# Kernel tuning notes

Measured on AMD Instinct MI355X. Metric: run time of the kernel, lower is better.

Reference implementation:

```python
import jax, jax.numpy as jnp
import numpy as np

W_PRIMAL, W_DUAL, W_STAT, W_COMP = 0.1, 0.1, 0.6, 0.2

B_ = 64
M_PER = 2048
N_PER = 2048
E = 8388608
SUM_M = B_ * M_PER
SUM_N = B_ * N_PER


def setup_inputs() -> dict:
    key = jax.random.key(0)
    k1, k2, k3, k4, k5, k6, k7 = jax.random.split(key, 7)
    return {
        "x_hat": jax.random.normal(k1, (SUM_N,), dtype=jnp.float32),
        "lam_hat": jax.random.normal(k2, (SUM_M,), dtype=jnp.float32),
        "edge_rows": jax.random.randint(k3, (E,), 0, SUM_M, dtype=jnp.int32),
        "edge_cols": jax.random.randint(k4, (E,), 0, SUM_N, dtype=jnp.int32),
        "edge_attr": jax.random.normal(k5, (E,), dtype=jnp.float32),
        "b_pad": jax.random.normal(k6, (B_, M_PER), dtype=jnp.float32),
        "c_pad": jax.random.normal(k7, (B_, N_PER), dtype=jnp.float32),
        "B": B_,
        "m_per": M_PER,
        "n_per": N_PER,
    }


def reference(x_hat, lam_hat, edge_rows, edge_cols, edge_attr, b_pad, c_pad, B, m_per, n_per):
    sum_m = B * m_per
    sum_n = B * n_per
    # masks are all-True (uniform instance sizes) -> b_pad[b_mask] == flatten
    b_cat = b_pad.reshape(-1).astype(jnp.float32)  # [sum_m]
    c_cat = c_pad.reshape(-1).astype(jnp.float32)  # [sum_n]

    x = x_hat.astype(jnp.float32)
    l = lam_hat.astype(jnp.float32)
    a = edge_attr.astype(jnp.float32)

    # SpMV via edge-list scatter-add: Ax and A^T lam
    Ax = jnp.zeros(sum_m, jnp.float32).at[edge_rows].add(a * x[edge_cols])
    ATlam = jnp.zeros(sum_n, jnp.float32).at[edge_cols].add(a * l[edge_rows])

    Ax_minus_b = Ax - b_cat
    primal_vec = jax.nn.relu(Ax_minus_b)
    dual_vec = jax.nn.relu(-l)
    stat_vec = ATlam + c_cat
    compl_vec = l * Ax_minus_b

    row_batch = jnp.repeat(jnp.arange(B, dtype=jnp.int32), m_per)  # [sum_m]
    col_batch = jnp.repeat(jnp.arange(B, dtype=jnp.int32), n_per)  # [sum_n]

    def seg_mean_sq(vec, seg, count):
        sums = jax.ops.segment_sum(vec * vec, seg, num_segments=B)
        return sums / jnp.float32(max(count, 1))

    loss_pr = seg_mean_sq(primal_vec, row_batch, m_per).sum()
    loss_du = seg_mean_sq(dual_vec, row_batch, m_per).sum()
    loss_st = seg_mean_sq(stat_vec, col_batch, n_per).sum()
    loss_cs = seg_mean_sq(compl_vec, row_batch, m_per).sum()

    total = (W_PRIMAL * loss_pr + W_DUAL * loss_du
             + W_STAT * loss_st + W_COMP * loss_cs) / jnp.float32(B)
    return total
```

## Files before the change

### kernel.cpp

```cpp
#include <hip/hip_runtime.h>
#include <stdint.h>

static constexpr int THREADS = 256;
static constexpr int SCAN_THREADS = 1024;
static constexpr int LOSS_BLOCKS = 256;
static constexpr int CHUNK = 32768;
static constexpr int REP_T = 32;

static constexpr int CM  = 16384;
static constexpr int CN  = 16384;
static constexpr int CSZ = CM + CN;
static constexpr int MAX_REP = 32;

typedef int   vint4   __attribute__((ext_vector_type(4)));
typedef float vfloat4 __attribute__((ext_vector_type(4)));

template <int REP>
__global__ __launch_bounds__(SCAN_THREADS) void kkt_scan2_t(
    const int* __restrict__ rows, const int* __restrict__ cols,
    const float* __restrict__ attr,
    const float* __restrict__ x, const float* __restrict__ lam,
    float* __restrict__ partial, int E, int NPr) {
  __shared__ float lds[CHUNK];
  const int q = blockIdx.x / REP;
  const int r = blockIdx.x % REP;
  const bool rowside = q < NPr;
  const unsigned base = (unsigned)((rowside ? q : q - NPr) * CHUNK);

  vfloat4* l4 = (vfloat4*)lds;
  for (int i = threadIdx.x; i < CHUNK / 4; i += SCAN_THREADS) l4[i] = (vfloat4)(0.0f);
  __syncthreads();

  long per = (((long)E + REP - 1) / REP + 3) & ~3L;
  long e0 = per * r;  if (e0 > E) e0 = E;
  long e1 = e0 + per; if (e1 > E) e1 = E;
  long n4 = (e1 - e0) >> 2;

  const vint4*   rows4 = (const vint4*)(rows + e0);
  const vint4*   cols4 = (const vint4*)(cols + e0);
  const vfloat4* attr4 = (const vfloat4*)(attr + e0);
  const int tid = threadIdx.x;

  if (rowside) {
    for (long qq = tid; qq < n4; qq += SCAN_THREADS) {
      vint4   rr = rows4[qq];
      vint4   cc = cols4[qq];
      vfloat4 aa = attr4[qq];
#define ROW_ACC(RR, CC, AA)                                                  \
      do {                                                                   \
        unsigned k = (unsigned)(RR) - base;                                  \
        if (k < (unsigned)CHUNK) unsafeAtomicAdd(&lds[k], (AA) * x[(CC)]);   \
      } while (0)
      ROW_ACC(rr.x, cc.x, aa.x);
      ROW_ACC(rr.y, cc.y, aa.y);
      ROW_ACC(rr.z, cc.z, aa.z);
      ROW_ACC(rr.w, cc.w, aa.w);
    }
    for (long i = e0 + (n4 << 2) + tid; i < e1; i += SCAN_THREADS) {
      int rv = rows[i], cv = cols[i];
      float a = attr[i];
      ROW_ACC(rv, cv, a);
    }
#undef ROW_ACC
  } else {
    for (long qq = tid; qq < n4; qq += SCAN_THREADS) {
      vint4   rr = rows4[qq];
      vint4   cc = cols4[qq];
      vfloat4 aa = attr4[qq];
#define COL_ACC(RR, CC, AA)                                                  \
      do {                                                                   \
        unsigned k = (unsigned)(CC) - base;                                  \
        if (k < (unsigned)CHUNK) unsafeAtomicAdd(&lds[k], (AA) * lam[(RR)]); \
      } while (0)
      COL_ACC(rr.x, cc.x, aa.x);
      COL_ACC(rr.y, cc.y, aa.y);
      COL_ACC(rr.z, cc.z, aa.z);
      COL_ACC(rr.w, cc.w, aa.w);
    }
    for (long i = e0 + (n4 << 2) + tid; i < e1; i += SCAN_THREADS) {
      int rv = rows[i], cv = cols[i];
      float a = attr[i];
      COL_ACC(rv, cv, a);
    }
#undef COL_ACC
  }

  __syncthreads();
  vfloat4* d4 = (vfloat4*)(partial + (size_t)blockIdx.x * CHUNK);
  for (int i = threadIdx.x; i < CHUNK / 4; i += SCAN_THREADS)
    __builtin_nontemporal_store(l4[i], d4 + i);
}

template <int REP>
__global__ __launch_bounds__(THREADS) void kkt_loss2_t(
    const float* __restrict__ partial,
    const float* __restrict__ bcat, const float* __restrict__ ccat,
    const float* __restrict__ lam, double* __restrict__ bacc,
    int sum_m, int sum_n, int NPr) {
  long idx = (long)blockIdx.x * THREADS + threadIdx.x;
  long stride = (long)gridDim.x * THREADS;
  long total4 = ((long)sum_m + sum_n) >> 2;
  long m4 = (long)sum_m >> 2;
  const size_t col_off = (size_t)NPr * REP * CHUNK;
  double pr = 0.0, du = 0.0, st = 0.0, cs = 0.0;
  for (long g = idx; g < total4; g += stride) {
    if (g < m4) {
      int ii = (int)(g << 2);
      int p = ii / CHUNK, j = ii & (CHUNK - 1);
      const float* b = partial + (size_t)(p * REP) * CHUNK + j;
      vfloat4 ax = (vfloat4)(0.0f);
#pragma unroll
      for (int s = 0; s < REP; ++s)
        ax += __builtin_nontemporal_load((const vfloat4*)(b + (size_t)s * CHUNK));
      vfloat4 bc = *(const vfloat4*)(bcat + ii);
      vfloat4 lv = *(const vfloat4*)(lam + ii);
#pragma unroll
      for (int t = 0; t < 4; ++t) {
        float d  = ax[t] - bc[t];
        float li = lv[t];
        float pp   = d > 0.0f ? d : 0.0f;
        float u    = li < 0.0f ? -li : 0.0f;
        float comp = li * d;
        pr += (double)pp * pp;
        du += (double)u * u;
        cs += (double)comp * comp;
      }
    } else {
      int ii = (int)((g - m4) << 2);
      int p = ii / CHUNK, j = ii & (CHUNK - 1);
      const float* b = partial + col_off + (size_t)(p * REP) * CHUNK + j;
      vfloat4 at = (vfloat4)(0.0f);
#pragma unroll
      for (int s = 0; s < REP; ++s)
        at += __builtin_nontemporal_load((const vfloat4*)(b + (size_t)s * CHUNK));
      vfloat4 cc = *(const vfloat4*)(ccat + ii);
#pragma unroll
      for (int t = 0; t < 4; ++t) {
        float sv = at[t] + cc[t];
        st += (double)sv * sv;
      }
    }
  }
  for (int off = 32; off > 0; off >>= 1) {
    pr += __shfl_down(pr, off);
    du += __shfl_down(du, off);
    st += __shfl_down(st, off);
    cs += __shfl_down(cs, off);
  }
  __shared__ double sred[THREADS / 64][4];
  const int wv = threadIdx.x >> 6;
  if ((threadIdx.x & 63) == 0) {
    sred[wv][0] = pr; sred[wv][1] = du; sred[wv][2] = st; sred[wv][3] = cs;
  }
  __syncthreads();
  if (threadIdx.x == 0) {
    double a0 = 0, a1 = 0, a2 = 0, a3 = 0;
#pragma unroll
    for (int w = 0; w < THREADS / 64; ++w) {
      a0 += sred[w][0]; a1 += sred[w][1]; a2 += sred[w][2]; a3 += sred[w][3];
    }
    bacc[(size_t)blockIdx.x * 4 + 0] = a0;
    bacc[(size_t)blockIdx.x * 4 + 1] = a1;
    bacc[(size_t)blockIdx.x * 4 + 2] = a2;
    bacc[(size_t)blockIdx.x * 4 + 3] = a3;
  }
}

__global__ __launch_bounds__(THREADS) void kkt_finalize_fast(
    const double* __restrict__ bacc, int nblk,
    const int* __restrict__ Bp, const int* __restrict__ mp,
    const int* __restrict__ np_, float* __restrict__ out) {
  double v0 = 0, v1 = 0, v2 = 0, v3 = 0;
  for (int i = threadIdx.x; i < nblk; i += THREADS) {
    v0 += bacc[(size_t)i * 4 + 0];
    v1 += bacc[(size_t)i * 4 + 1];
    v2 += bacc[(size_t)i * 4 + 2];
    v3 += bacc[(size_t)i * 4 + 3];
  }
  for (int off = 32; off > 0; off >>= 1) {
    v0 += __shfl_down(v0, off);
    v1 += __shfl_down(v1, off);
    v2 += __shfl_down(v2, off);
    v3 += __shfl_down(v3, off);
  }
  __shared__ double sred[THREADS / 64][4];
  const int wv = threadIdx.x >> 6;
  if ((threadIdx.x & 63) == 0) {
    sred[wv][0] = v0; sred[wv][1] = v1; sred[wv][2] = v2; sred[wv][3] = v3;
  }
  __syncthreads();
  if (threadIdx.x == 0) {
    double a0 = 0, a1 = 0, a2 = 0, a3 = 0;
#pragma unroll
    for (int w = 0; w < THREADS / 64; ++w) {
      a0 += sred[w][0]; a1 += sred[w][1]; a2 += sred[w][2]; a3 += sred[w][3];
    }
    double m = (double)mp[0];
    double n = (double)np_[0];
    double B = (double)Bp[0];
    out[0] = (float)((0.1 * (a0 + a1) / m + 0.6 * a2 / n + 0.2 * a3 / m) / B);
  }
}

__global__ void kkt_init(double* __restrict__ acc, float* __restrict__ out) {
  int t = threadIdx.x;
  if (t < 4) acc[t] = 0.0;
  if (t == 0) out[0] = 0.0f;
}

__global__ __launch_bounds__(SCAN_THREADS) void kkt_scan_dyn(
    const int* __restrict__ rows, const int* __restrict__ cols,
    const float* __restrict__ attr,
    const float* __restrict__ x, const float* __restrict__ lam,
    float* __restrict__ partial, int E, int REP) {
  __shared__ float lds[CSZ];
  const int p = blockIdx.x / REP;
  const int r = blockIdx.x % REP;
  const int baseM = p * CM;
  const int baseN = p * CN;
  vfloat4* l4 = (vfloat4*)lds;
  for (int i = threadIdx.x; i < CSZ / 4; i += SCAN_THREADS) l4[i] = (vfloat4)(0.0f);
  __syncthreads();
  long per = (((long)E + REP - 1) / REP + 3) & ~3L;
  long e0 = per * r;  if (e0 > E) e0 = E;
  long e1 = e0 + per; if (e1 > E) e1 = E;
  int  n4 = (int)((e1 - e0) >> 2);
  const vint4*   rows4 = (const vint4*)(rows + e0);
  const vint4*   cols4 = (const vint4*)(cols + e0);
  const vfloat4* attr4 = (const vfloat4*)(attr + e0);
#define EDGE_ACC(RR, CC, AA)                                                 \
  do {                                                                       \
    unsigned mm = (unsigned)((RR) - baseM);                                  \
    if (mm < (unsigned)CM) unsafeAtomicAdd(&lds[mm], (AA) * x[(CC)]);        \
    unsigned nn = (unsigned)((CC) - baseN);                                  \
    if (nn < (unsigned)CN) unsafeAtomicAdd(&lds[CM + nn], (AA) * lam[(RR)]); \
  } while (0)
  for (int i = threadIdx.x; i < n4; i += SCAN_THREADS) {
    vint4 rr = rows4[i]; vint4 cc = cols4[i]; vfloat4 aa = attr4[i];
    EDGE_ACC(rr.x, cc.x, aa.x);
    EDGE_ACC(rr.y, cc.y, aa.y);
    EDGE_ACC(rr.z, cc.z, aa.z);
    EDGE_ACC(rr.w, cc.w, aa.w);
  }
  for (long i = e0 + ((long)n4 << 2) + threadIdx.x; i < e1; i += SCAN_THREADS) {
    int rr = rows[i], cc = cols[i];
    float aa = attr[i];
    EDGE_ACC(rr, cc, aa);
  }
#undef EDGE_ACC
  __syncthreads();
  vfloat4* d4 = (vfloat4*)(partial + (size_t)(p * REP + r) * CSZ);
  for (int i = threadIdx.x; i < CSZ / 4; i += SCAN_THREADS) d4[i] = l4[i];
}

__global__ __launch_bounds__(THREADS) void kkt_loss_dyn(
    const float* __restrict__ partial,
    const float* __restrict__ bcat, const float* __restrict__ ccat,
    const float* __restrict__ lam, double* __restrict__ acc,
    int sum_m, int sum_n, int REP) {
  int idx = blockIdx.x * blockDim.x + threadIdx.x;
  int stride = gridDim.x * blockDim.x;
  double pr = 0.0, du = 0.0, st = 0.0, cs = 0.0;
  for (int i = idx; i < sum_m; i += stride) {
    int p = i / CM, j = i - p * CM;
    const float* base = partial + (size_t)(p * REP) * CSZ + j;
    float ax = 0.0f;
    for (int rr = 0; rr < REP; ++rr) ax += base[(size_t)rr * CSZ];
    float d  = ax - bcat[i];
    float li = lam[i];
    float pp   = d > 0.0f ? d : 0.0f;
    float u    = li < 0.0f ? -li : 0.0f;
    float comp = li * d;
    pr += (double)pp * pp;
    du += (double)u * u;
    cs += (double)comp * comp;
  }
  for (int i = idx; i < sum_n; i += stride) {
    int p = i / CN, j = i - p * CN;
    const float* base = partial + (size_t)(p * REP) * CSZ + CM + j;
    float at = 0.0f;
    for (int rr = 0; rr < REP; ++rr) at += base[(size_t)rr * CSZ];
    float s = at + ccat[i];
    st += (double)s * s;
  }
  for (int off = 32; off > 0; off >>= 1) {
    pr += __shfl_down(pr, off);
    du += __shfl_down(du, off);
    st += __shfl_down(st, off);
    cs += __shfl_down(cs, off);
  }
  if ((threadIdx.x & 63) == 0) {
    unsafeAtomicAdd(&acc[0], pr);
    unsafeAtomicAdd(&acc[1], du);
    unsafeAtomicAdd(&acc[2], st);
    unsafeAtomicAdd(&acc[3], cs);
  }
}

__global__ void kkt_finalize(const double* __restrict__ acc,
                             const int* __restrict__ Bp,
                             const int* __restrict__ mp,
                             const int* __restrict__ np_,
                             float* __restrict__ out) {
  double m = (double)mp[0];
  double n = (double)np_[0];
  double B = (double)Bp[0];
  double total =
      (0.1 * (acc[0] + acc[1]) / m + 0.6 * acc[2] / n + 0.2 * acc[3] / m) / B;
  out[0] = (float)total;
}

extern "C" void kernel_launch(void* const* d_in, const int* in_sizes, int n_in,
                              void* d_out, int out_size, void* d_ws, size_t ws_size,
                              hipStream_t stream) {
  const float* x    = (const float*)d_in[0];
  const float* lam  = (const float*)d_in[1];
  const int*   rows = (const int*)d_in[2];
  const int*   cols = (const int*)d_in[3];
  const float* attr = (const float*)d_in[4];
  const float* bcat = (const float*)d_in[5];
  const float* ccat = (const float*)d_in[6];
  const int*   Bp   = (const int*)d_in[7];
  const int*   mp   = (const int*)d_in[8];
  const int*   np_  = (const int*)d_in[9];

  const int sum_n = in_sizes[0];
  const int sum_m = in_sizes[1];
  const int E     = in_sizes[2];

  char*   ws   = (char*)d_ws;
  double* acc  = (double*)ws;
  double* bacc = (double*)(ws + 256);
  float*  buf  = (float*)(ws + 256 + LOSS_BLOCKS * 4 * sizeof(double));
  float*  out  = (float*)d_out;

  const int NPr = (sum_m + CHUNK - 1) / CHUNK;
  const int NPc = (sum_n + CHUNK - 1) / CHUNK;
  const int NQ  = NPr + NPc;

  const size_t head = 256 + (size_t)LOSS_BLOCKS * 4 * sizeof(double);
  size_t avail = ws_size > head ? ws_size - head : 0;
  const size_t need_t = (size_t)NQ * REP_T * CHUNK * sizeof(float);

  const bool vec_ok = ((sum_m & 3) == 0) && ((sum_n & 3) == 0);

  if (avail >= need_t && vec_ok) {
    kkt_scan2_t<REP_T><<<NQ * REP_T, SCAN_THREADS, 0, stream>>>(
        rows, cols, attr, x, lam, buf, E, NPr);
    kkt_loss2_t<REP_T><<<LOSS_BLOCKS, THREADS, 0, stream>>>(
        buf, bcat, ccat, lam, bacc, sum_m, sum_n, NPr);
    kkt_finalize_fast<<<1, THREADS, 0, stream>>>(bacc, LOSS_BLOCKS, Bp, mp,
                                                 np_, out);
  } else {
    float* fbuf = (float*)(ws + 64);
    const int NPm = (sum_m + CM - 1) / CM;
    const int NPn = (sum_n + CN - 1) / CN;
    const int NP  = NPm > NPn ? NPm : NPn;
    size_t favail = ws_size > 64 ? ws_size - 64 : 0;
    int REP = (int)(favail / ((size_t)NP * CSZ * sizeof(float)));
    if (REP > MAX_REP) REP = MAX_REP;
    if (REP < 1) REP = 1;
    kkt_init<<<1, 64, 0, stream>>>(acc, out);
    kkt_scan_dyn<<<NP * REP, SCAN_THREADS, 0, stream>>>(rows, cols, attr, x,
                                                        lam, fbuf, E, REP);
    int lw = sum_m > sum_n ? sum_m : sum_n;
    int lb = (lw + THREADS - 1) / THREADS;
    if (lb > 1024) lb = 1024;
    kkt_loss_dyn<<<lb, THREADS, 0, stream>>>(fbuf, bcat, ccat, lam, acc,
                                             sum_m, sum_n, REP);
    kkt_finalize<<<1, 1, 0, stream>>>(acc, Bp, mp, np_, out);
  }
}
```

Baseline: 122.9 us.

## Precompute per-edge products once before the LDS scatter scan

Adds a pre-pass kernel that computes a*x[col] and a*lam[row] for every edge once and writes them to workspace arrays. The scan kernel then reads only an index stream and a value stream, so each of the many replicated chunk blocks no longer re-reads three edge arrays and does random gathers. This costs an extra pass over the edges and two extra E-sized writes, plus more workspace. The loss kernel block count is also raised.

```diff
diff --git a/kernel.cpp b/kernel.cpp
--- a/kernel.cpp
+++ b/kernel.cpp
@@ -3,7 +3,7 @@
 
 static constexpr int THREADS = 256;
 static constexpr int SCAN_THREADS = 1024;
-static constexpr int LOSS_BLOCKS = 256;
+static constexpr int LOSS_BLOCKS = 512;
 static constexpr int CHUNK = 32768;
 static constexpr int REP_T = 32;
 
@@ -15,17 +15,50 @@
 typedef int   vint4   __attribute__((ext_vector_type(4)));
 typedef float vfloat4 __attribute__((ext_vector_type(4)));
 
-template <int REP>
-__global__ __launch_bounds__(SCAN_THREADS) void kkt_scan2_t(
+__global__ __launch_bounds__(THREADS) void kkt_pre(
     const int* __restrict__ rows, const int* __restrict__ cols,
     const float* __restrict__ attr,
     const float* __restrict__ x, const float* __restrict__ lam,
+    float* __restrict__ g, float* __restrict__ h, int E) {
+  long idx = (long)blockIdx.x * THREADS + threadIdx.x;
+  long stride = (long)gridDim.x * THREADS;
+  long n4 = (long)E >> 2;
+  const vint4*   rows4 = (const vint4*)rows;
+  const vint4*   cols4 = (const vint4*)cols;
+  const vfloat4* attr4 = (const vfloat4*)attr;
+  vfloat4* g4 = (vfloat4*)g;
+  vfloat4* h4 = (vfloat4*)h;
+  for (long q = idx; q < n4; q += stride) {
+    vint4   rr = rows4[q];
+    vint4   cc = cols4[q];
+    vfloat4 aa = attr4[q];
+    vfloat4 gg, hh;
+    gg.x = aa.x * x[cc.x];  hh.x = aa.x * lam[rr.x];
+    gg.y = aa.y * x[cc.y];  hh.y = aa.y * lam[rr.y];
+    gg.z = aa.z * x[cc.z];  hh.z = aa.z * lam[rr.z];
+    gg.w = aa.w * x[cc.w];  hh.w = aa.w * lam[rr.w];
+    __builtin_nontemporal_store(gg, g4 + q);
+    __builtin_nontemporal_store(hh, h4 + q);
+  }
+  for (long i = (n4 << 2) + idx; i < E; i += stride) {
+    float a = attr[i];
+    g[i] = a * x[cols[i]];
+    h[i] = a * lam[rows[i]];
+  }
+}
+
+template <int REP>
+__global__ __launch_bounds__(SCAN_THREADS) void kkt_scan3_t(
+    const int* __restrict__ rows, const int* __restrict__ cols,
+    const float* __restrict__ g, const float* __restrict__ h,
     float* __restrict__ partial, int E, int NPr) {
   __shared__ float lds[CHUNK];
   const int q = blockIdx.x / REP;
   const int r = blockIdx.x % REP;
   const bool rowside = q < NPr;
   const unsigned base = (unsigned)((rowside ? q : q - NPr) * CHUNK);
+  const int*   idxs = rowside ? rows : cols;
+  const float* vals = rowside ? g : h;
 
   vfloat4* l4 = (vfloat4*)lds;
   for (int i = threadIdx.x; i < CHUNK / 4; i += SCAN_THREADS) l4[i] = (vfloat4)(0.0f);
@@ -36,53 +69,25 @@
   long e1 = e0 + per; if (e1 > E) e1 = E;
   long n4 = (e1 - e0) >> 2;
 
-  const vint4*   rows4 = (const vint4*)(rows + e0);
-  const vint4*   cols4 = (const vint4*)(cols + e0);
-  const vfloat4* attr4 = (const vfloat4*)(attr + e0);
+  const vint4*   idx4 = (const vint4*)(idxs + e0);
+  const vfloat4* val4 = (const vfloat4*)(vals + e0);
   const int tid = threadIdx.x;
 
-  if (rowside) {
-    for (long qq = tid; qq < n4; qq += SCAN_THREADS) {
-      vint4   rr = rows4[qq];
-      vint4   cc = cols4[qq];
-      vfloat4 aa = attr4[qq];
-#define ROW_ACC(RR, CC, AA)                                                  \
-      do {                                                                   \
-        unsigned k = (unsigned)(RR) - base;                                  \
-        if (k < (unsigned)CHUNK) unsafeAtomicAdd(&lds[k], (AA) * x[(CC)]);   \
-      } while (0)
-      ROW_ACC(rr.x, cc.x, aa.x);
-      ROW_ACC(rr.y, cc.y, aa.y);
-      ROW_ACC(rr.z, cc.z, aa.z);
-      ROW_ACC(rr.w, cc.w, aa.w);
-    }
-    for (long i = e0 + (n4 << 2) + tid; i < e1; i += SCAN_THREADS) {
-      int rv = rows[i], cv = cols[i];
-      float a = attr[i];
-      ROW_ACC(rv, cv, a);
-    }
-#undef ROW_ACC
-  } else {
-    for (long qq = tid; qq < n4; qq += SCAN_THREADS) {
-      vint4   rr = rows4[qq];
-      vint4   cc = cols4[qq];
-      vfloat4 aa = attr4[qq];
-#define COL_ACC(RR, CC, AA)                                                  \
-      do {                                                                   \
-        unsigned k = (unsigned)(CC) - base;                                  \
-        if (k < (unsigned)CHUNK) unsafeAtomicAdd(&lds[k], (AA) * lam[(RR)]); \
-      } while (0)
-      COL_ACC(rr.x, cc.x, aa.x);
-      COL_ACC(rr.y, cc.y, aa.y);
-      COL_ACC(rr.z, cc.z, aa.z);
-      COL_ACC(rr.w, cc.w, aa.w);
-    }
-    for (long i = e0 + (n4 << 2) + tid; i < e1; i += SCAN_THREADS) {
-      int rv = rows[i], cv = cols[i];
-      float a = attr[i];
-      COL_ACC(rv, cv, a);
-    }
-#undef COL_ACC
+  for (long qq = tid; qq < n4; qq += SCAN_THREADS) {
+    vint4   ii = idx4[qq];
+    vfloat4 vv = val4[qq];
+    unsigned k0 = (unsigned)ii.x - base;
+    unsigned k1 = (unsigned)ii.y - base;
+    unsigned k2 = (unsigned)ii.z - base;
+    unsigned k3 = (unsigned)ii.w - base;
+    if (k0 < (unsigned)CHUNK) unsafeAtomicAdd(&lds[k0], vv.x);
+    if (k1 < (unsigned)CHUNK) unsafeAtomicAdd(&lds[k1], vv.y);
+    if (k2 < (unsigned)CHUNK) unsafeAtomicAdd(&lds[k2], vv.z);
+    if (k3 < (unsigned)CHUNK) unsafeAtomicAdd(&lds[k3], vv.w);
+  }
+  for (long i = e0 + (n4 << 2) + tid; i < e1; i += SCAN_THREADS) {
+    unsigned k = (unsigned)idxs[i] - base;
+    if (k < (unsigned)CHUNK) unsafeAtomicAdd(&lds[k], vals[i]);
   }
 
   __syncthreads();
@@ -103,9 +108,9 @@
   long m4 = (long)sum_m >> 2;
   const size_t col_off = (size_t)NPr * REP * CHUNK;
   double pr = 0.0, du = 0.0, st = 0.0, cs = 0.0;
-  for (long g = idx; g < total4; g += stride) {
-    if (g < m4) {
-      int ii = (int)(g << 2);
+  for (long gq = idx; gq < total4; gq += stride) {
+    if (gq < m4) {
+      int ii = (int)(gq << 2);
       int p = ii / CHUNK, j = ii & (CHUNK - 1);
       const float* b = partial + (size_t)(p * REP) * CHUNK + j;
       vfloat4 ax = (vfloat4)(0.0f);
@@ -126,7 +131,7 @@
         cs += (double)comp * comp;
       }
     } else {
-      int ii = (int)((g - m4) << 2);
+      int ii = (int)((gq - m4) << 2);
       int p = ii / CHUNK, j = ii & (CHUNK - 1);
       const float* b = partial + col_off + (size_t)(p * REP) * CHUNK + j;
       vfloat4 at = (vfloat4)(0.0f);
@@ -200,6 +205,71 @@
     double B = (double)Bp[0];
     out[0] = (float)((0.1 * (a0 + a1) / m + 0.6 * a2 / n + 0.2 * a3 / m) / B);
   }
+}
+
+template <int REP>
+__global__ __launch_bounds__(SCAN_THREADS) void kkt_scan2_t(
+    const int* __restrict__ rows, const int* __restrict__ cols,
+    const float* __restrict__ attr,
+    const float* __restrict__ x, const float* __restrict__ lam,
+    float* __restrict__ partial, int E, int NPr) {
+  __shared__ float lds[CHUNK];
+  const int q = blockIdx.x / REP;
+  const int r = blockIdx.x % REP;
+  const bool rowside = q < NPr;
+  const unsigned base = (unsigned)((rowside ? q : q - NPr) * CHUNK);
+  vfloat4* l4 = (vfloat4*)lds;
+  for (int i = threadIdx.x; i < CHUNK / 4; i += SCAN_THREADS) l4[i] = (vfloat4)(0.0f);
+  __syncthreads();
+  long per = (((long)E + REP - 1) / REP + 3) & ~3L;
+  long e0 = per * r;  if (e0 > E) e0 = E;
+  long e1 = e0 + per; if (e1 > E) e1 = E;
+  long n4 = (e1 - e0) >> 2;
+  const vint4*   rows4 = (const vint4*)(rows + e0);
+  const vint4*   cols4 = (const vint4*)(cols + e0);
+  const vfloat4* attr4 = (const vfloat4*)(attr + e0);
+  const int tid = threadIdx.x;
+  if (rowside) {
+    for (long qq = tid; qq < n4; qq += SCAN_THREADS) {
+      vint4 rr = rows4[qq]; vint4 cc = cols4[qq]; vfloat4 aa = attr4[qq];
+#define ROW_ACC(RR, CC, AA)                                                  \
+      do {                                                                   \
+        unsigned k = (unsigned)(RR) - base;                                  \
+        if (k < (unsigned)CHUNK) unsafeAtomicAdd(&lds[k], (AA) * x[(CC)]);   \
+      } while (0)
+      ROW_ACC(rr.x, cc.x, aa.x);
+      ROW_ACC(rr.y, cc.y, aa.y);
+      ROW_ACC(rr.z, cc.z, aa.z);
+      ROW_ACC(rr.w, cc.w, aa.w);
+    }
+    for (long i = e0 + (n4 << 2) + tid; i < e1; i += SCAN_THREADS) {
+      int rv = rows[i], cv = cols[i]; float a = attr[i];
+      ROW_ACC(rv, cv, a);
+    }
+#undef ROW_ACC
+  } else {
+    for (long qq = tid; qq < n4; qq += SCAN_THREADS) {
+      vint4 rr = rows4[qq]; vint4 cc = cols4[qq]; vfloat4 aa = attr4[qq];
+#define COL_ACC(RR, CC, AA)                                                  \
+      do {                                                                   \
+        unsigned k = (unsigned)(CC) - base;                                  \
+        if (k < (unsigned)CHUNK) unsafeAtomicAdd(&lds[k], (AA) * lam[(RR)]); \
+      } while (0)
+      COL_ACC(rr.x, cc.x, aa.x);
+      COL_ACC(rr.y, cc.y, aa.y);
+      COL_ACC(rr.z, cc.z, aa.z);
+      COL_ACC(rr.w, cc.w, aa.w);
+    }
+    for (long i = e0 + (n4 << 2) + tid; i < e1; i += SCAN_THREADS) {
+      int rv = rows[i], cv = cols[i]; float a = attr[i];
+      COL_ACC(rv, cv, a);
+    }
+#undef COL_ACC
+  }
+  __syncthreads();
+  vfloat4* d4 = (vfloat4*)(partial + (size_t)blockIdx.x * CHUNK);
+  for (int i = threadIdx.x; i < CHUNK / 4; i += SCAN_THREADS)
+    __builtin_nontemporal_store(l4[i], d4 + i);
 }
 
 __global__ void kkt_init(double* __restrict__ acc, float* __restrict__ out) {
@@ -331,7 +401,6 @@
   char*   ws   = (char*)d_ws;
   double* acc  = (double*)ws;
   double* bacc = (double*)(ws + 256);
-  float*  buf  = (float*)(ws + 256 + LOSS_BLOCKS * 4 * sizeof(double));
   float*  out  = (float*)d_out;
 
   const int NPr = (sum_m + CHUNK - 1) / CHUNK;
@@ -339,12 +408,29 @@
   const int NQ  = NPr + NPc;
 
   const size_t head = 256 + (size_t)LOSS_BLOCKS * 4 * sizeof(double);
+  const size_t part_bytes = (size_t)NQ * REP_T * CHUNK * sizeof(float);
+  const size_t gsz = ((size_t)E + 3 & ~(size_t)3) * sizeof(float);
+
+  float* buf = (float*)(ws + head);
+  float* g   = (float*)(ws + head + part_bytes);
+  float* h   = g + (gsz / sizeof(float));
+
   size_t avail = ws_size > head ? ws_size - head : 0;
-  const size_t need_t = (size_t)NQ * REP_T * CHUNK * sizeof(float);
-
   const bool vec_ok = ((sum_m & 3) == 0) && ((sum_n & 3) == 0);
-
-  if (avail >= need_t && vec_ok) {
+  const size_t need1 = part_bytes + 2 * gsz;
+  const size_t need2 = part_bytes;
+
+  if (avail >= need1 && vec_ok) {
+    int pb = (int)(((long)E / 4 + THREADS - 1) / THREADS);
+    if (pb > 2048) pb = 2048;
+    kkt_pre<<<pb, THREADS, 0, stream>>>(rows, cols, attr, x, lam, g, h, E);
+    kkt_scan3_t<REP_T><<<NQ * REP_T, SCAN_THREADS, 0, stream>>>(
+        rows, cols, g, h, buf, E, NPr);
+    kkt_loss2_t<REP_T><<<LOSS_BLOCKS, THREADS, 0, stream>>>(
+        buf, bcat, ccat, lam, bacc, sum_m, sum_n, NPr);
+    kkt_finalize_fast<<<1, THREADS, 0, stream>>>(bacc, LOSS_BLOCKS, Bp, mp,
+                                                 np_, out);
+  } else if (avail >= need2 && vec_ok) {
     kkt_scan2_t<REP_T><<<NQ * REP_T, SCAN_THREADS, 0, stream>>>(
         rows, cols, attr, x, lam, buf, E, NPr);
     kkt_loss2_t<REP_T><<<LOSS_BLOCKS, THREADS, 0, stream>>>(
```

Measured after the change: 186.5 us. +51.7%, slower.
